# Kernel optimization log

Hardware: AMD Instinct MI355X
Metric: run time of the kernel (lower is better)

The kernel has to match this reference:

```python
import jax, jax.numpy as jnp
import numpy as np
from jax import lax

V_WORD, D_WORD = 50000, 300
V_CHAR, D_CHAR = 128, 50
FILTER_NUM, KSIZE = 4, 3
OUT_CH = D_CHAR * FILTER_NUM  # 200
SENT, BATCH, WLEN = 256, 64, 16


def setup_inputs() -> dict:
    key = jax.random.key(0)
    k1, k2, k3, k4, k5, k6 = jax.random.split(key, 6)
    words = jax.random.randint(k1, (SENT, BATCH), 0, V_WORD, dtype=jnp.int32)
    chars = jax.random.randint(k2, (BATCH, SENT, WLEN), 0, V_CHAR, dtype=jnp.int32)
    W_word = jax.random.normal(k3, (V_WORD, D_WORD), dtype=jnp.float32) * 0.1
    W_char = jax.random.normal(k4, (V_CHAR, D_CHAR), dtype=jnp.float32) * 0.1
    conv_w = jax.random.normal(k5, (OUT_CH, D_CHAR, KSIZE), dtype=jnp.float32) * 0.1
    conv_b = jax.random.normal(k6, (OUT_CH,), dtype=jnp.float32) * 0.1
    return {"words": words, "chars": chars, "W_word": W_word, "W_char": W_char,
            "conv_w": conv_w, "conv_b": conv_b}


def reference(words, chars, W_word, W_char, conv_w, conv_b):
    # word embedding: [S, B, Dw]  (dropout layers are identity in eval mode)
    word_emb = W_word[words]
    # char embedding: [B, S, L, Dc]
    char_emb = W_char[chars]
    B, S, L, Dc = char_emb.shape
    # batch all words into one conv call: [B*S, Dc, L]
    x = char_emb.reshape(B * S, L, Dc).transpose(0, 2, 1)
    y = lax.conv_general_dilated(
        x, conv_w, window_strides=(1,), padding='VALID',
        dimension_numbers=('NCH', 'OIH', 'NCH'))  # [B*S, OUT_CH, L-K+1]
    y = y + conv_b[None, :, None]
    pooled = jnp.max(y, axis=2).reshape(B, S, -1)  # [B, S, OUT_CH]
    char_feat = pooled.transpose(1, 0, 2)          # [S, B, OUT_CH]
    return jnp.concatenate([word_emb, char_feat], axis=2)  # [S, B, Dw+OUT_CH]
```

## Files before the change

### kernel.cpp

```cpp
#include <hip/hip_runtime.h>

#define SENT    256
#define BATCH   64
#define WLEN    16
#define D_WORDE 300
#define D_CHARE 50
#define OUT_CH  200
#define KSIZE   3
#define NPOS    14
#define D_OUT   500
#define NWORDS  (SENT * BATCH)

#define KPAD      192
#define MPAD      208
#define CHARP_U16 (129 * 64)
#define WO_U16    (MPAD * KPAD)
#define WS_NEED   ((size_t)(CHARP_U16 + WO_U16) * 2)

#define WPB         16
#define TILE_U16    (WPB * 1024)
#define CONV_BLOCKS (NWORDS / WPB)

typedef short  short8  __attribute__((ext_vector_type(8)));
typedef ushort ushort8 __attribute__((ext_vector_type(8)));
typedef float  float4v __attribute__((ext_vector_type(4)));

#define GLOAD16(SRC, DST)                                                     \
    __builtin_amdgcn_global_load_lds(                                         \
        (const __attribute__((address_space(1))) void*)(SRC),                 \
        (__attribute__((address_space(3))) void*)(DST), 16, 0, 0)

__device__ __forceinline__ ushort f2bf(float f) {
    unsigned u = __float_as_uint(f);
    u = (u + 0x7FFFu + ((u >> 16) & 1u)) >> 16;
    return (ushort)u;
}

__global__ void prep_kernel(const float* __restrict__ W_char,
                            const float* __restrict__ conv_w,
                            const float* __restrict__ conv_b,
                            ushort* __restrict__ ws) {
    int j = blockIdx.x * 256 + threadIdx.x;
    if (j < CHARP_U16) {
        int r = j >> 6, c = j & 63;
        ushort v = 0;
        if (r < 128) {
            if (c < D_CHARE)      v = f2bf(W_char[r * D_CHARE + c]);
            else if (c == 63)     v = 0x3F80;
        }
        ws[j] = v;
    }
    int j2 = j - CHARP_U16;
    if (j2 >= 0 && j2 < WO_U16) {
        int o = j2 / KPAD, kg = j2 - o * KPAD;
        int kk = kg >> 6, c = kg & 63;
        float v = 0.f;
        if (o < OUT_CH) {
            if (c < D_CHARE)      v = conv_w[o * (D_CHARE * KSIZE) + c * KSIZE + kk];
            else if (kg == 191)   v = conv_b[o];
        }
        ws[CHARP_U16 + j2] = f2bf(v);
    }
}

__device__ __forceinline__ float4v fmax4(float4v a, float4v b) {
    float4v r;
    r[0] = fmaxf(a[0], b[0]); r[1] = fmaxf(a[1], b[1]);
    r[2] = fmaxf(a[2], b[2]); r[3] = fmaxf(a[3], b[3]);
    return r;
}

__device__ __forceinline__ short8 lda(const ushort* __restrict__ tile,
                                      int l15, int row, int g) {
    int pos = g ^ (row & 7) ^ (l15 & 7);
    return *(const short8*)&tile[l15 * 1024 + row * 64 + (pos << 3)];
}

template <int NT>
__device__ __forceinline__ void conv_ploop(int tbase, int lane, int l15, int lg,
                                           const ushort* __restrict__ tile,
                                           const ushort* __restrict__ WO,
                                           float* __restrict__ out, int block0) {
    short8 B[NT][6];
    #pragma unroll
    for (int i = 0; i < NT; i++) {
        int col = (tbase + i) * 16 + l15;
        #pragma unroll
        for (int s = 0; s < 6; s++)
            B[i][s] = *(const short8*)&WO[col * KPAD + s * 32 + lg * 8];
    }

    short8 a0 = lda(tile, l15, 0, lg),     a1 = lda(tile, l15, 0, 4 + lg);
    short8 a2 = lda(tile, l15, 1, lg),     a3 = lda(tile, l15, 1, 4 + lg);
    short8 a4 = lda(tile, l15, 2, lg),     a5 = lda(tile, l15, 2, 4 + lg);

    float4v mx[NT];
    #pragma unroll
    for (int p = 0; p < NPOS; p++) {
        float4v acc[NT];
        #pragma unroll
        for (int i = 0; i < NT; i++) acc[i] = (float4v){0, 0, 0, 0};
        #pragma unroll
        for (int i = 0; i < NT; i++) acc[i] = __builtin_amdgcn_mfma_f32_16x16x32_bf16(a0, B[i][0], acc[i], 0, 0, 0);
        #pragma unroll
        for (int i = 0; i < NT; i++) acc[i] = __builtin_amdgcn_mfma_f32_16x16x32_bf16(a1, B[i][1], acc[i], 0, 0, 0);
        #pragma unroll
        for (int i = 0; i < NT; i++) acc[i] = __builtin_amdgcn_mfma_f32_16x16x32_bf16(a2, B[i][2], acc[i], 0, 0, 0);
        #pragma unroll
        for (int i = 0; i < NT; i++) acc[i] = __builtin_amdgcn_mfma_f32_16x16x32_bf16(a3, B[i][3], acc[i], 0, 0, 0);
        #pragma unroll
        for (int i = 0; i < NT; i++) acc[i] = __builtin_amdgcn_mfma_f32_16x16x32_bf16(a4, B[i][4], acc[i], 0, 0, 0);
        #pragma unroll
        for (int i = 0; i < NT; i++) acc[i] = __builtin_amdgcn_mfma_f32_16x16x32_bf16(a5, B[i][5], acc[i], 0, 0, 0);

        #pragma unroll
        for (int i = 0; i < NT; i++) mx[i] = (p == 0) ? acc[i] : fmax4(mx[i], acc[i]);

        if (p < NPOS - 1) {
            a0 = a2; a1 = a3; a2 = a4; a3 = a5;
            a4 = lda(tile, l15, p + 3, lg);
            a5 = lda(tile, l15, p + 3, 4 + lg);
        }
    }

    #pragma unroll
    for (int i = 0; i < NT; i++) {
        int col = (tbase + i) * 16 + l15;
        if (col < OUT_CH) {
            #pragma unroll
            for (int j = 0; j < 4; j++)
                out[(size_t)(block0 + lg * 4 + j) * D_OUT + D_WORDE + col] = mx[i][j];
        }
    }
}

__global__ void __launch_bounds__(512)
fused_kernel(const int* __restrict__ words, const int* __restrict__ chars,
             const float* __restrict__ W_word, const ushort* __restrict__ ws,
             float* __restrict__ out) {
    __shared__ __align__(16) ushort tile[TILE_U16];

    const int tid  = threadIdx.x;
    const int lane = tid & 63;
    const int wave = tid >> 6;
    const int l15  = lane & 15;
    const int lg   = lane >> 4;

    const ushort* __restrict__ charP = ws;
    const ushort* __restrict__ WO    = ws + CHARP_U16;
    const int block0 = blockIdx.x * WPB;

    #pragma unroll
    for (int ww = 0; ww < 2; ww++) {
        const int wl = wave * 2 + ww;
        const int m  = block0 + wl;
        const int* __restrict__ cbase = chars + ((m & 63) * SENT + (m >> 6)) * WLEN;
        const int srcg = (lane & 7) ^ ((lane >> 3) & 7) ^ (wl & 7);
        #pragma unroll
        for (int s = 0; s < 2; s++) {
            const int idv = cbase[s * 8 + (lane >> 3)];
            GLOAD16(charP + idv * 64 + (srcg << 3), &tile[wl * 1024 + s * 512]);
        }
    }
    __syncthreads();

    if (wave < 6) {
        conv_ploop<2>(2 * wave, lane, l15, lg, tile, WO, out, block0);
    } else if (wave == 6) {
        conv_ploop<1>(12, lane, l15, lg, tile, WO, out, block0);
    } else {
        const bool tail = lane < (75 - 64);
        #pragma unroll 1
        for (int r4 = 0; r4 < 4; r4++) {
            const int m0 = block0 + r4 * 4;
            float4v e0[4], e1[4];
            #pragma unroll
            for (int j = 0; j < 4; j++) {
                const float4v* __restrict__ src =
                    (const float4v*)(W_word + (size_t)words[m0 + j] * D_WORDE);
                e0[j] = src[lane];
                e1[j] = tail ? src[64 + lane] : (float4v){0, 0, 0, 0};
            }
            #pragma unroll
            for (int j = 0; j < 4; j++) {
                float4v* __restrict__ dst = (float4v*)(out + (size_t)(m0 + j) * D_OUT);
                dst[lane] = e0[j];
                if (tail) dst[64 + lane] = e1[j];
            }
        }
    }
}

__global__ void __launch_bounds__(256)
word_emb_kernel(const int* __restrict__ words, const float* __restrict__ W_word,
                float* __restrict__ out) {
    int wave = threadIdx.x >> 6, lane = threadIdx.x & 63;
    int m = blockIdx.x * 4 + wave;
    int idx = words[m];
    const float* __restrict__ src = W_word + (size_t)idx * D_WORDE;
    float* __restrict__ dst = out + (size_t)m * D_OUT;
    for (int j = lane; j < D_WORDE; j += 64) dst[j] = src[j];
}

__global__ void __launch_bounds__(256)
char_conv_f32_kernel(const int* __restrict__ chars, const float* __restrict__ W_char,
                     const float* __restrict__ conv_w, const float* __restrict__ conv_b,
                     float* __restrict__ out) {
    __shared__ __align__(16) float xs[D_CHARE * WLEN];
    __shared__ int ids[WLEN];
    int m = blockIdx.x, s = m >> 6, b = m & 63, tid = threadIdx.x;
    if (tid < WLEN) ids[tid] = chars[(b * SENT + s) * WLEN + tid];
    __syncthreads();
    for (int e = tid; e < D_CHARE * WLEN; e += 256) {
        int c = e >> 4, l = e & 15;
        xs[e] = W_char[ids[l] * D_CHARE + c];
    }
    __syncthreads();
    if (tid < OUT_CH) {
        float acc[NPOS];
        #pragma unroll
        for (int p = 0; p < NPOS; p++) acc[p] = 0.f;
        const float4* xs4 = (const float4*)xs;
        for (int c = 0; c < D_CHARE; c++) {
            float4 a0 = xs4[c*4+0], a1 = xs4[c*4+1], a2 = xs4[c*4+2], a3 = xs4[c*4+3];
            float xr[WLEN] = {a0.x,a0.y,a0.z,a0.w, a1.x,a1.y,a1.z,a1.w,
                              a2.x,a2.y,a2.z,a2.w, a3.x,a3.y,a3.z,a3.w};
            #pragma unroll
            for (int k = 0; k < KSIZE; k++) {
                float wv = conv_w[tid * (D_CHARE * KSIZE) + c * KSIZE + k];
                #pragma unroll
                for (int p = 0; p < NPOS; p++) acc[p] = fmaf(wv, xr[p + k], acc[p]);
            }
        }
        float mx = acc[0];
        #pragma unroll
        for (int p = 1; p < NPOS; p++) mx = fmaxf(mx, acc[p]);
        out[(size_t)m * D_OUT + D_WORDE + tid] = mx + conv_b[tid];
    }
}

extern "C" void kernel_launch(void* const* d_in, const int* in_sizes, int n_in,
                              void* d_out, int out_size, void* d_ws, size_t ws_size,
                              hipStream_t stream) {
    const int*   words  = (const int*)d_in[0];
    const int*   chars  = (const int*)d_in[1];
    const float* W_word = (const float*)d_in[2];
    const float* W_char = (const float*)d_in[3];
    const float* conv_w = (const float*)d_in[4];
    const float* conv_b = (const float*)d_in[5];
    float* out = (float*)d_out;

    if (ws_size >= WS_NEED) {
        ushort* ws = (ushort*)d_ws;
        hipLaunchKernelGGL(prep_kernel,
                           dim3((CHARP_U16 + WO_U16 + 255) / 256), dim3(256), 0, stream,
                           W_char, conv_w, conv_b, ws);
        hipLaunchKernelGGL(fused_kernel, dim3(CONV_BLOCKS), dim3(512), 0, stream,
                           words, chars, W_word, ws, out);
    } else {
        hipLaunchKernelGGL(word_emb_kernel, dim3(NWORDS / 4), dim3(256), 0, stream,
                           words, W_word, out);
        hipLaunchKernelGGL(char_conv_f32_kernel, dim3(NWORDS), dim3(256), 0, stream,
                           chars, W_char, conv_w, conv_b, out);
    }
}
```

Before: 33.20 us.

## Stage conv outputs in LDS for coalesced stores and rebalance embedding copy across waves

Conv results are written to a shared-memory buffer instead of scattered directly to global memory. After a barrier, all waves write them back as contiguous row segments. The word-embedding copy is split so wave 6, which has less conv work, handles 4 rows and wave 7 handles 12. This aims to coalesce the strided output stores and balance load across waves, at the cost of 16KB extra LDS and an extra barrier.

```diff
diff --git a/kernel.cpp b/kernel.cpp
--- a/kernel.cpp
+++ b/kernel.cpp
@@ -19,6 +19,7 @@
 
 #define WPB         16
 #define TILE_U16    (WPB * 1024)
+#define CBUF_STRIDE 256
 #define CONV_BLOCKS (NWORDS / WPB)
 
 typedef short  short8  __attribute__((ext_vector_type(8)));
@@ -80,7 +81,7 @@
 __device__ __forceinline__ void conv_ploop(int tbase, int lane, int l15, int lg,
                                            const ushort* __restrict__ tile,
                                            const ushort* __restrict__ WO,
-                                           float* __restrict__ out, int block0) {
+                                           float* __restrict__ cbuf) {
     short8 B[NT][6];
     #pragma unroll
     for (int i = 0; i < NT; i++) {
@@ -126,10 +127,33 @@
     #pragma unroll
     for (int i = 0; i < NT; i++) {
         int col = (tbase + i) * 16 + l15;
-        if (col < OUT_CH) {
-            #pragma unroll
-            for (int j = 0; j < 4; j++)
-                out[(size_t)(block0 + lg * 4 + j) * D_OUT + D_WORDE + col] = mx[i][j];
+        #pragma unroll
+        for (int j = 0; j < 4; j++)
+            cbuf[(lg * 4 + j) * CBUF_STRIDE + col] = mx[i][j];
+    }
+}
+
+__device__ __forceinline__ void emb_rows(int block0, int r0, int cnt, int lane,
+                                         const int* __restrict__ words,
+                                         const float* __restrict__ W_word,
+                                         float* __restrict__ out) {
+    const bool tail = lane < (75 - 64);
+    #pragma unroll 1
+    for (int r4 = 0; r4 < cnt; r4 += 4) {
+        const int m0 = block0 + r0 + r4;
+        float4v e0[4], e1[4];
+        #pragma unroll
+        for (int j = 0; j < 4; j++) {
+            const float4v* __restrict__ src =
+                (const float4v*)(W_word + (size_t)words[m0 + j] * D_WORDE);
+            e0[j] = src[lane];
+            e1[j] = tail ? src[64 + lane] : (float4v){0, 0, 0, 0};
+        }
+        #pragma unroll
+        for (int j = 0; j < 4; j++) {
+            float4v* __restrict__ dst = (float4v*)(out + (size_t)(m0 + j) * D_OUT);
+            dst[lane] = e0[j];
+            if (tail) dst[64 + lane] = e1[j];
         }
     }
 }
@@ -139,6 +163,7 @@
              const float* __restrict__ W_word, const ushort* __restrict__ ws,
              float* __restrict__ out) {
     __shared__ __align__(16) ushort tile[TILE_U16];
+    __shared__ __align__(16) float  cbuf[WPB * CBUF_STRIDE];
 
     const int tid  = threadIdx.x;
     const int lane = tid & 63;
@@ -165,29 +190,24 @@
     __syncthreads();
 
     if (wave < 6) {
-        conv_ploop<2>(2 * wave, lane, l15, lg, tile, WO, out, block0);
+        conv_ploop<2>(2 * wave, lane, l15, lg, tile, WO, cbuf);
     } else if (wave == 6) {
-        conv_ploop<1>(12, lane, l15, lg, tile, WO, out, block0);
+        conv_ploop<1>(12, lane, l15, lg, tile, WO, cbuf);
+        emb_rows(block0, 12, 4, lane, words, W_word, out);
     } else {
-        const bool tail = lane < (75 - 64);
-        #pragma unroll 1
-        for (int r4 = 0; r4 < 4; r4++) {
-            const int m0 = block0 + r4 * 4;
-            float4v e0[4], e1[4];
-            #pragma unroll
-            for (int j = 0; j < 4; j++) {
-                const float4v* __restrict__ src =
-                    (const float4v*)(W_word + (size_t)words[m0 + j] * D_WORDE);
-                e0[j] = src[lane];
-                e1[j] = tail ? src[64 + lane] : (float4v){0, 0, 0, 0};
-            }
-            #pragma unroll
-            for (int j = 0; j < 4; j++) {
-                float4v* __restrict__ dst = (float4v*)(out + (size_t)(m0 + j) * D_OUT);
-                dst[lane] = e0[j];
-                if (tail) dst[64 + lane] = e1[j];
-            }
-        }
+        emb_rows(block0, 0, 12, lane, words, W_word, out);
+    }
+    __syncthreads();
+
+    #pragma unroll
+    for (int rr = 0; rr < 2; rr++) {
+        const int r = wave * 2 + rr;
+        const float* __restrict__ src = &cbuf[r * CBUF_STRIDE];
+        float* __restrict__ dst = out + (size_t)(block0 + r) * D_OUT + D_WORDE;
+        dst[lane]       = src[lane];
+        dst[64 + lane]  = src[64 + lane];
+        dst[128 + lane] = src[128 + lane];
+        if (lane < 8) dst[192 + lane] = src[192 + lane];
     }
 }
 
```

After: 33.91 us. 2.1% more time.
